# Kernel tuning notes

Hardware: AMD Instinct MI355X
Metric: run time of the kernel (lower is better)

Reference implementation:

```python
import jax, jax.numpy as jnp
import numpy as np

N = 15872   # number of predictions (31 * 512)
D = 129     # 128 image features + 1 objectness score
H = 128     # block MLP hidden width
IN = 2 * D + 1  # neighbor feats + main feats + add_info (IoU)
NUM_BLOCKS = 2


def _lin(k, fi, fo):
    return jax.random.normal(k, (fi, fo), jnp.float32) / np.sqrt(fi).astype(np.float32)


def setup_inputs() -> dict:
    key = jax.random.key(0)
    ks = jax.random.split(key, 24)
    # ragged neighborhood structure: mean size 16, exactly E = 16*N edges
    sizes = (np.arange(N) % 31) + 1
    E = int(sizes.sum())  # 253952
    rng = np.random.default_rng(0)
    nbr_idx = rng.integers(0, N, size=E).astype(np.int32)
    self_idx = np.repeat(np.arange(N, dtype=np.int32), sizes)  # sorted segment ids

    inp = {
        "interpolated": jax.random.normal(ks[0], (N, D), jnp.float32),
        "add_info": jax.random.uniform(ks[1], (E, 1), dtype=jnp.float32),
        "neighborhood_sizes": jnp.asarray(sizes, jnp.int32),
        "neighborhoods_indexes": jnp.asarray(nbr_idx),
        "self_indexes": jnp.asarray(self_idx),
    }
    # two (block, output) model pairs
    inp["b0_W1"] = _lin(ks[2], IN, H); inp["b0_b1"] = jnp.zeros((H,), jnp.float32)
    inp["b0_W2"] = _lin(ks[3], H, H);  inp["b0_b2"] = jnp.zeros((H,), jnp.float32)
    inp["b0_Wo"] = _lin(ks[4], H, D); inp["b0_bo"] = jnp.zeros((D,), jnp.float32)
    inp["b1_W1"] = _lin(ks[5], IN, H); inp["b1_b1"] = jnp.zeros((H,), jnp.float32)
    inp["b1_W2"] = _lin(ks[6], H, H);  inp["b1_b2"] = jnp.zeros((H,), jnp.float32)
    inp["b1_Wo"] = _lin(ks[7], H, D); inp["b1_bo"] = jnp.zeros((D,), jnp.float32)
    # final layers: 129 -> 64 -> 1
    inp["f_W1"] = _lin(ks[8], D, 64); inp["f_b1"] = jnp.zeros((64,), jnp.float32)
    inp["f_W2"] = _lin(ks[9], 64, 1); inp["f_b2"] = jnp.zeros((1,), jnp.float32)
    return inp


def _lnms_forward(interpolated, add_info, params, nbr_idx, self_idx):
    # params: list of (W1, b1, W2, b2, Wo, bo) per block, plus (fW1, fb1, fW2, fb2)
    for (W1, b1, W2, b2, Wo, bo) in params[:-1]:
        nbr = interpolated[nbr_idx]    # (E, D) gather of neighbor representations
        main = interpolated[self_idx]  # (E, D) gather of owning prediction
        x = jnp.concatenate([nbr, main, add_info], axis=1)  # (E, 2D+1)
        h = jax.nn.relu(x @ W1 + b1)
        h = jax.nn.relu(h @ W2 + b2)   # (E, H) processed neighborhoods
        # ragged per-neighborhood max pool (segments are contiguous/sorted)
        pooled = jax.ops.segment_max(h, self_idx, num_segments=N,
                                     indices_are_sorted=True)  # (N, H)
        block_output = pooled @ Wo + bo  # (N, D)
        interpolated = interpolated + block_output  # residual scatter-update
    fW1, fb1, fW2, fb2 = params[-1]
    return jax.nn.relu(interpolated @ fW1 + fb1) @ fW2 + fb2  # (N, 1)


def reference(interpolated, add_info,
              b0_W1, b0_b1, b0_W2, b0_b2, b0_Wo, b0_bo,
              b1_W1, b1_b1, b1_W2, b1_b2, b1_Wo, b1_bo,
              f_W1, f_b1, f_W2, f_b2,
              neighborhood_sizes, neighborhoods_indexes, self_indexes):
    params = [
        (b0_W1, b0_b1, b0_W2, b0_b2, b0_Wo, b0_bo),
        (b1_W1, b1_b1, b1_W2, b1_b2, b1_Wo, b1_bo),
        (f_W1, f_b1, f_W2, f_b2),
    ]
    return _lnms_forward(interpolated, add_info, params,
                         neighborhoods_indexes, self_indexes)
```

## Files before the change

kernel.cpp:

```cpp
#include <hip/hip_runtime.h>

#define NSEG 15872
#define DD 129
#define HH 128
#define NTILE (NSEG / 16)

typedef __attribute__((ext_vector_type(8))) short s16x8;
typedef __attribute__((ext_vector_type(4))) short s16x4;
typedef __attribute__((ext_vector_type(4))) float f32x4;
typedef __attribute__((ext_vector_type(16))) float f32x16;
typedef __attribute__((ext_vector_type(4))) unsigned u32x4;

__device__ __forceinline__ unsigned short f2bf(float x) {
  union { float f; unsigned u; } c; c.f = x;
  unsigned r = c.u + 0x7FFFu + ((c.u >> 16) & 1u);
  return (unsigned short)(r >> 16);
}
__device__ __forceinline__ float bf2f(unsigned short v) {
  union { unsigned u; float f; } c; c.u = ((unsigned)v) << 16; return c.f;
}

__device__ __forceinline__ void packB8(short* out, int idx8, const float* W,
                                       int N, int ld, int ncols, int kLimit,
                                       int rowBase) {
  const int n = (idx8 >> 3) % N;
  const int g = idx8 / (8 * N);
  s16x8 o;
#pragma unroll
  for (int i = 0; i < 8; ++i) {
    const int row = g * 8 + i;
    float v = 0.f;
    if (row < kLimit && n < ncols) v = W[(long)(rowBase + row) * ld + n];
    o[i] = (short)f2bf(v);
  }
  *(s16x8*)(out + idx8) = o;
}

__device__ __forceinline__ void packA1T8(short* out, int idx8, const float* W1) {
  const int unit = idx8 >> 3;
  const int lane = unit & 63;
  const int blk = unit >> 6;
  const int Mblk = blk / 10, ks = blk % 10;
  const int m = Mblk * 32 + (lane & 31);
  const int k0 = ks * 16 + ((lane >> 5) << 3);
  s16x8 o;
#pragma unroll
  for (int i = 0; i < 8; ++i) {
    const int k = k0 + i;
    o[i] = (short)((k < DD) ? f2bf(W1[(long)k * HH + m]) : 0);
  }
  *(s16x8*)(out + idx8) = o;
}

__device__ __forceinline__ void packB2T8(short* out, int idx8, const float* W2) {
  const int unit = idx8 >> 3;
  const int lane = unit & 63;
  const int blk = unit >> 6;
  const int ks = blk >> 2, nb = blk & 3;
  const int n = nb * 32 + (lane & 31);
  const int k0 = ks * 16 + ((lane >> 5) << 3);
  s16x8 o;
#pragma unroll
  for (int i = 0; i < 8; ++i)
    o[i] = (short)f2bf(W2[(long)(k0 + i) * HH + n]);
  *(s16x8*)(out + idx8) = o;
}

#define PACK_IDS 161792
#define TAB_IDS (NSEG * 160)
#define PACKV (PACK_IDS / 8)
#define TABV (TAB_IDS / 8)
#define PTBLK ((PACKV + TABV) / 256)
#define HMBLK (NTILE / 4)
__global__ __launch_bounds__(256) void pack_tab_kernel(
    const float* __restrict__ interp, unsigned short* __restrict__ tab,
    const float* __restrict__ W1b0, const float* __restrict__ W1b1,
    const float* __restrict__ W2b0, const float* __restrict__ W2b1,
    const float* __restrict__ Wob0, const float* __restrict__ Wob1,
    const float* __restrict__ fW1, short* __restrict__ PA1,
    short* __restrict__ PB2, short* __restrict__ PWo,
    short* __restrict__ PW1m, short* __restrict__ PfW1,
    const float* __restrict__ b1, float* __restrict__ Hm,
    const int* __restrict__ sizes, int* __restrict__ offs) {
  __shared__ short w1s[20480];
  const int bid = blockIdx.x;
  if (bid == PTBLK + HMBLK) {
    int* sums = (int*)w1s;
    const int t = threadIdx.x;
    const int base = t * (NSEG / 256);
    int s = 0;
#pragma unroll 8
    for (int i = 0; i < NSEG / 256; ++i) s += sizes[base + i];
    sums[t] = s;
    __syncthreads();
    for (int d = 1; d < 256; d <<= 1) {
      int u = (t >= d) ? sums[t - d] : 0;
      __syncthreads();
      sums[t] += u;
      __syncthreads();
    }
    int a = sums[t] - s;
#pragma unroll 8
    for (int i = 0; i < NSEG / 256; ++i) {
      const int sz = sizes[base + i];
      offs[base + i] = a;
      a += sz;
    }
    if (t == 255) offs[NSEG] = a;
    return;
  }
  if (bid >= PTBLK) {
    const int hb = bid - PTBLK;
    for (int u = threadIdx.x; u < 2560; u += 256)
      packB8(w1s, u * 8, W1b0, 128, 128, 128, 129, 129);
    __syncthreads();
    const int lane = threadIdx.x & 63, w = threadIdx.x >> 6;
    const int lk = lane >> 4, n16 = lane & 15;
    const int tile = hb * 4 + w;
    const float* arow = interp + (long)(tile * 16 + n16) * DD;
    s16x8 A[5];
#pragma unroll
    for (int ks = 0; ks < 5; ++ks) {
      s16x8 o;
#pragma unroll
      for (int i = 0; i < 8; ++i) {
        const int k = ks * 32 + lk * 8 + i;
        o[i] = (short)((k < DD) ? f2bf(arow[k]) : 0);
      }
      A[ks] = o;
    }
    f32x4 C[8];
#pragma unroll
    for (int nf = 0; nf < 8; ++nf) C[nf] = (f32x4){0.f, 0.f, 0.f, 0.f};
#pragma unroll
    for (int ks = 0; ks < 5; ++ks)
#pragma unroll
      for (int nf = 0; nf < 8; ++nf) {
        const s16x8 b = *(const s16x8*)(w1s + (((ks * 4 + lk) * 128) + nf * 16 + n16) * 8);
        C[nf] = __builtin_amdgcn_mfma_f32_16x16x32_bf16(A[ks], b, C[nf], 0, 0, 0);
      }
#pragma unroll
    for (int nf = 0; nf < 8; ++nf) {
      const float bv = b1[nf * 16 + n16];
#pragma unroll
      for (int r = 0; r < 4; ++r)
        Hm[(long)(tile * 16 + lk * 4 + r) * HH + nf * 16 + n16] = C[nf][r] + bv;
    }
    return;
  }
  int vid = bid * 256 + threadIdx.x;
  if (vid < PACKV) {
    int idx = vid * 8;
    if (idx < 40960) {
      packA1T8(PA1 + (idx / 20480) * 20480, idx % 20480,
               (idx < 20480) ? W1b0 : W1b1);
      return;
    }
    idx -= 40960;
    if (idx < 32768) {
      packB2T8(PB2 + (idx / 16384) * 16384, idx % 16384,
               (idx < 16384) ? W2b0 : W2b1);
      return;
    }
    idx -= 32768;
    if (idx < 36864) {
      packB8(PWo + (idx / 18432) * 18432, idx % 18432,
             (idx < 18432) ? Wob0 : Wob1, 144, 129, 129, 128, 0);
      return;
    }
    idx -= 36864;
    if (idx < 40960) {
      packB8(PW1m + (idx / 20480) * 20480, idx % 20480,
             (idx < 20480) ? W1b0 : W1b1, 128, 128, 128, 129, 129);
      return;
    }
    idx -= 40960;
    packB8(PfW1, idx, fW1, 64, 64, 64, 129, 0);
    return;
  }
  vid -= PACKV;
  if (vid < TABV) {
    const int n = vid / 20;
    const int g = vid - n * 20;
    s16x8 o = (s16x8){0, 0, 0, 0, 0, 0, 0, 0};
    if (g < 16) {
      const float* src = interp + (long)n * DD + g * 8;
#pragma unroll
      for (int i = 0; i < 8; ++i) o[i] = (short)f2bf(src[i]);
    } else if (g == 16) {
      o[0] = (short)f2bf(interp[(long)n * DD + 128]);
    }
    *(s16x8*)(tab + (long)vid * 8) = o;
  }
}

__device__ __forceinline__ int pairEdge(int row, int oLo, int sLo, int oHi,
                                        int sHi) {
  int e = (row < sLo) ? (oLo + row) : (oHi + row - sLo);
  if (row >= sLo + sHi) e = oHi + sHi - 1;
  return e;
}

struct PairMeta {
  int segLo, segHi, oLo, sLo, oHi, sHi;
};

__device__ __forceinline__ void loadMeta(int p, PairMeta& M,
                                         const int* __restrict__ offs) {
  M.segLo = p;
  M.segHi = NSEG - 1 - p;
  M.oLo = offs[M.segLo]; M.sLo = offs[M.segLo + 1] - M.oLo;
  M.oHi = offs[M.segHi]; M.sHi = offs[M.segHi + 1] - M.oHi;
}

__device__ __forceinline__ void prefetchEdge(
    const PairMeta& M, int c, const int* __restrict__ nbrIdx,
    const float* __restrict__ iou, int n32, int& nbrow, float& io) {
  const int grow = (c << 5) + n32;
  const int e = pairEdge(grow, M.oLo, M.sLo, M.oHi, M.sHi);
  nbrow = nbrIdx[e];
  io = iou[e];
}

__device__ __forceinline__ void prefetchHm(
    const PairMeta& M, const float* __restrict__ Hm, int n32,
    float* hmLo, float* hmHi) {
#pragma unroll
  for (int q = 0; q < 4; ++q) {
    hmLo[q] = Hm[(long)M.segLo * HH + q * 32 + n32];
    hmHi[q] = Hm[(long)M.segHi * HH + q * 32 + n32];
  }
}

__device__ __forceinline__ void gatherX(const unsigned short* __restrict__ tab,
                                        int nbrow, int half, s16x8* X) {
  const unsigned short* ar = tab + (long)nbrow * 160;
#pragma unroll
  for (int ks = 0; ks < 9; ++ks)
    X[ks] = *(const s16x8*)(ar + ks * 16 + half * 8);
}

__device__ __forceinline__ void gemm1Phase(
    const PairMeta& M, int c, const s16x8* X, float io,
    const short* __restrict__ As1, const float* wvT,
    const float* hmLo, const float* hmHi,
    int lane, int half, int n32, s16x8* A2) {
  const int grow = (c << 5) + n32;
  const short oneBf = (short)0x3F80;
  s16x8 bb = (s16x8){0, 0, 0, 0, 0, 0, 0, 0};
  if (half == 0) {
    const bool lo = grow < M.sLo;
    bb[0] = lo ? oneBf : (short)0;
    bb[1] = bb[0];
    bb[2] = lo ? (short)0 : oneBf;
    bb[3] = bb[2];
    bb[4] = (short)f2bf(io);
  }
#pragma unroll
  for (int Mblk = 0; Mblk < 4; ++Mblk) {
    f32x16 C;
#pragma unroll
    for (int i = 0; i < 16; ++i) C[i] = 0.f;
#pragma unroll
    for (int ks = 0; ks < 9; ++ks) {
      const s16x8 a = *(const s16x8*)(As1 + ((Mblk * 10 + ks) * 64 + lane) * 8);
      C = __builtin_amdgcn_mfma_f32_32x32x16_bf16(a, X[ks], C, 0, 0, 0);
    }
    s16x8 ab = (s16x8){0, 0, 0, 0, 0, 0, 0, 0};
    if (half == 0) {
      const unsigned short p0 = f2bf(hmLo[Mblk]);
      ab[0] = (short)p0;
      ab[1] = (short)f2bf(hmLo[Mblk] - bf2f(p0));
      const unsigned short p1 = f2bf(hmHi[Mblk]);
      ab[2] = (short)p1;
      ab[3] = (short)f2bf(hmHi[Mblk] - bf2f(p1));
      ab[4] = (short)f2bf(wvT[Mblk]);
    }
    C = __builtin_amdgcn_mfma_f32_32x32x16_bf16(ab, bb, C, 0, 0, 0);
    unsigned wv[8];
#pragma unroll
    for (int j = 0; j < 8; ++j) {
      const float lo = fmaxf(C[2 * j], 0.f);
      const float hi = fmaxf(C[2 * j + 1], 0.f);
      asm("v_cvt_pk_bf16_f32 %0, %1, %2" : "=v"(wv[j]) : "v"(lo), "v"(hi));
    }
    asm("v_permlane32_swap_b32 %0, %1" : "+v"(wv[0]), "+v"(wv[2]));
    asm("v_permlane32_swap_b32 %0, %1" : "+v"(wv[1]), "+v"(wv[3]));
    asm("v_permlane32_swap_b32 %0, %1" : "+v"(wv[4]), "+v"(wv[6]));
    asm("v_permlane32_swap_b32 %0, %1" : "+v"(wv[5]), "+v"(wv[7]));
    union { u32x4 u; s16x8 s; } q0, q1;
    q0.u = (u32x4){wv[0], wv[1], wv[2], wv[3]};
    q1.u = (u32x4){wv[4], wv[5], wv[6], wv[7]};
    A2[2 * Mblk] = q0.s;
    A2[2 * Mblk + 1] = q1.s;
  }
}

__device__ __forceinline__ void gemm2Phase(
    const PairMeta& M, int c, const s16x8* A2, const short* __restrict__ Bs2,
    int lane, int half, int n32, float* mxLo, float* mxHi) {
#pragma unroll
  for (int nb = 0; nb < 4; ++nb) {
    f32x16 D;
#pragma unroll
    for (int i = 0; i < 16; ++i) D[i] = 0.f;
#pragma unroll
    for (int ks = 0; ks < 8; ++ks) {
      const s16x8 b = *(const s16x8*)(Bs2 + ((ks * 4 + nb) * 64 + lane) * 8);
      D = __builtin_amdgcn_mfma_f32_32x32x16_bf16(A2[ks], b, D, 0, 0, 0);
    }
#pragma unroll
    for (int reg = 0; reg < 16; ++reg) {
      const int rrow = (reg & 3) + 8 * (reg >> 2) + 4 * half;
      const int gr = (c << 5) + rrow;
      const float v = D[reg];
      if (gr < M.sLo) mxLo[nb] = fmaxf(mxLo[nb], v);
      else            mxHi[nb] = fmaxf(mxHi[nb], v);
    }
  }
}

__global__ __launch_bounds__(512, 2) void edge_kernel(
    const unsigned short* __restrict__ tab, const short* __restrict__ PA1,
    const short* __restrict__ PB2, const float* __restrict__ W1,
    const float* __restrict__ Hm, const float* __restrict__ iou,
    const int* __restrict__ nbrIdx, const int* __restrict__ offs,
    const float* __restrict__ b2, unsigned short* __restrict__ pooled) {
  extern __shared__ __align__(16) char smem[];
  short* As1 = (short*)smem;
  short* Bs2 = (short*)(smem + 40960);
  {
    const f32x4* s1 = (const f32x4*)PA1;
    f32x4* d1 = (f32x4*)As1;
    for (int i = threadIdx.x; i < 2560; i += 512) d1[i] = s1[i];
    const f32x4* s2 = (const f32x4*)PB2;
    f32x4* d2 = (f32x4*)Bs2;
    for (int i = threadIdx.x; i < 2048; i += 512) d2[i] = s2[i];
  }
  __syncthreads();

  const int lane = threadIdx.x & 63;
  const int w = __builtin_amdgcn_readfirstlane(threadIdx.x >> 6);
  const int half = lane >> 5, n32 = lane & 31;

  float b2v[4], wvT[4];
#pragma unroll
  for (int q = 0; q < 4; ++q) {
    b2v[q] = b2[q * 32 + n32];
    wvT[q] = W1[258 * HH + q * 32 + n32];
  }

  const int wid = (blockIdx.x << 3) + w;
  const int nw = gridDim.x << 3;
  const int npairs = NSEG >> 1;

  if (wid >= npairs) return;

  PairMeta M, M1, M2;
  int nb1, nb2;
  float io, io1, io2;
  float hmLo[4], hmHi[4];
  s16x8 X[9];
  loadMeta(wid, M, offs);
  {
    int nb0;
    prefetchEdge(M, 0, nbrIdx, iou, n32, nb0, io);
    gatherX(tab, nb0, half, X);
  }
  prefetchHm(M, Hm, n32, hmLo, hmHi);
  if (wid + nw < npairs) {
    loadMeta(wid + nw, M1, offs);
    prefetchEdge(M1, 0, nbrIdx, iou, n32, nb1, io1);
  }

  int p = wid;
  for (;;) {
    const int pn1 = p + nw, pn2 = p + 2 * nw;
    const bool h1 = pn1 < npairs, h2 = pn2 < npairs;
    s16x8 A2[8];
    gemm1Phase(M, 0, X, io, As1, wvT, hmLo, hmHi, lane, half, n32, A2);
    const bool small = (M.sLo + M.sHi) <= 32;
    if (small && h1) {
      gatherX(tab, nb1, half, X);
      prefetchHm(M1, Hm, n32, hmLo, hmHi);
      if (h2) {
        loadMeta(pn2, M2, offs);
        prefetchEdge(M2, 0, nbrIdx, iou, n32, nb2, io2);
      }
    }
    float mxLo[4], mxHi[4];
#pragma unroll
    for (int q = 0; q < 4; ++q) { mxLo[q] = -3.4e38f; mxHi[q] = -3.4e38f; }
    gemm2Phase(M, 0, A2, Bs2, lane, half, n32, mxLo, mxHi);
    if (!small) {
      const int nchunk = (M.sLo + M.sHi + 31) >> 5;
      for (int c = 1; c < nchunk; ++c) {
        int nbf; float iof;
        prefetchEdge(M, c, nbrIdx, iou, n32, nbf, iof);
        gatherX(tab, nbf, half, X);
        gemm1Phase(M, c, X, iof, As1, wvT, hmLo, hmHi, lane, half, n32, A2);
        gemm2Phase(M, c, A2, Bs2, lane, half, n32, mxLo, mxHi);
      }
      if (h1) {
        gatherX(tab, nb1, half, X);
        prefetchHm(M1, Hm, n32, hmLo, hmHi);
        if (h2) {
          loadMeta(pn2, M2, offs);
          prefetchEdge(M2, 0, nbrIdx, iou, n32, nb2, io2);
        }
      }
    }
#pragma unroll
    for (int nb = 0; nb < 4; ++nb) {
      float lo = fmaxf(mxLo[nb], __shfl_xor(mxLo[nb], 32, 64));
      float hi = fmaxf(mxHi[nb], __shfl_xor(mxHi[nb], 32, 64));
      if (half == 0) {
        pooled[(long)M.segLo * HH + nb * 32 + n32] = f2bf(fmaxf(lo + b2v[nb], 0.f));
        pooled[(long)M.segHi * HH + nb * 32 + n32] = f2bf(fmaxf(hi + b2v[nb], 0.f));
      }
    }
    if (!h1) break;
    M = M1; io = io1;
    if (h2) { M1 = M2; nb1 = nb2; io1 = io2; }
    p = pn1;
  }
}

template <int NEXT>
__global__ __launch_bounds__(256) void resout_kernel(
    const unsigned short* __restrict__ pooled, const short* __restrict__ PWo,
    const float* __restrict__ bo, const float* __restrict__ resIn,
    float* __restrict__ resOut, unsigned short* __restrict__ tab,
    const short* __restrict__ PW1mN, const float* __restrict__ b1n,
    float* __restrict__ HmOut,
    const short* __restrict__ PfW1, const float* __restrict__ fb1,
    const float* __restrict__ fW2, const float* __restrict__ fb2,
    float* __restrict__ outFinal) {
  __shared__ short stS[4][16 * 168];
  const int lane = threadIdx.x & 63, w = threadIdx.x >> 6;
  const int lk = lane >> 4, n16 = lane & 15;
  short* st = stS[w];

  {
    const int row = lane >> 2, c0 = 129 + (lane & 3) * 8;
#pragma unroll
    for (int i = 0; i < 8; ++i) st[row * 168 + c0 + i] = 0;
  }

  const int tile = blockIdx.x * 4 + w;
  const unsigned short* arow = pooled + (long)(tile * 16 + n16) * HH;
  s16x8 A[4];
#pragma unroll
  for (int ks = 0; ks < 4; ++ks) A[ks] = *(const s16x8*)(arow + ks * 32 + lk * 8);
  f32x4 C[9];
#pragma unroll
  for (int nf = 0; nf < 9; ++nf) C[nf] = (f32x4){0.f, 0.f, 0.f, 0.f};
#pragma unroll
  for (int ks = 0; ks < 4; ++ks)
#pragma unroll
    for (int nf = 0; nf < 9; ++nf) {
      const s16x8 b = *(const s16x8*)(PWo + (((ks * 4 + lk) * 144) + nf * 16 + n16) * 8);
      C[nf] = __builtin_amdgcn_mfma_f32_16x16x32_bf16(A[ks], b, C[nf], 0, 0, 0);
    }

#pragma unroll
  for (int nf = 0; nf < 8; ++nf) {
    const int col = nf * 16 + n16;
    const float bov = bo[col];
#pragma unroll
    for (int r = 0; r < 4; ++r) {
      const int row = lk * 4 + r;
      const long node = tile * 16 + row;
      const float res = resIn[node * DD + col] + bov + C[nf][r];
      if (NEXT) {
        resOut[node * DD + col] = res;
        tab[node * 160 + col] = f2bf(res);
      }
      st[row * 168 + col] = (short)f2bf(res);
    }
  }
  if (n16 == 0) {
#pragma unroll
    for (int r = 0; r < 4; ++r) {
      const int row = lk * 4 + r;
      const long node = tile * 16 + row;
      const float res = resIn[node * DD + 128] + bo[128] + C[8][r];
      if (NEXT) {
        resOut[node * DD + 128] = res;
        tab[node * 160 + 128] = f2bf(res);
      }
      st[row * 168 + 128] = (short)f2bf(res);
    }
  }

  s16x8 A5[5];
#pragma unroll
  for (int ks = 0; ks < 5; ++ks)
    A5[ks] = *(const s16x8*)(st + n16 * 168 + ks * 32 + lk * 8);

  if (NEXT) {
    f32x4 H[8];
#pragma unroll
    for (int nf = 0; nf < 8; ++nf) H[nf] = (f32x4){0.f, 0.f, 0.f, 0.f};
#pragma unroll
    for (int ks = 0; ks < 5; ++ks)
#pragma unroll
      for (int nf = 0; nf < 8; ++nf) {
        const s16x8 b = *(const s16x8*)(PW1mN + (((ks * 4 + lk) * 128) + nf * 16 + n16) * 8);
        H[nf] = __builtin_amdgcn_mfma_f32_16x16x32_bf16(A5[ks], b, H[nf], 0, 0, 0);
      }
#pragma unroll
    for (int nf = 0; nf < 8; ++nf) {
      const float bv = b1n[nf * 16 + n16];
#pragma unroll
      for (int r = 0; r < 4; ++r)
        HmOut[(long)(tile * 16 + lk * 4 + r) * HH + nf * 16 + n16] = H[nf][r] + bv;
    }
  } else {
    f32x4 Ch[4];
#pragma unroll
    for (int nf = 0; nf < 4; ++nf) Ch[nf] = (f32x4){0.f, 0.f, 0.f, 0.f};
#pragma unroll
    for (int ks = 0; ks < 5; ++ks)
#pragma unroll
      for (int nf = 0; nf < 4; ++nf) {
        const s16x8 b = *(const s16x8*)(PfW1 + (((ks * 4 + lk) * 64) + nf * 16 + n16) * 8);
        Ch[nf] = __builtin_amdgcn_mfma_f32_16x16x32_bf16(A5[ks], b, Ch[nf], 0, 0, 0);
      }
    float b1v[4], w2v[4];
#pragma unroll
    for (int nf = 0; nf < 4; ++nf) {
      b1v[nf] = fb1[nf * 16 + n16];
      w2v[nf] = fW2[nf * 16 + n16];
    }
#pragma unroll
    for (int r = 0; r < 4; ++r) {
      float s = 0.f;
#pragma unroll
      for (int nf = 0; nf < 4; ++nf)
        s += fmaxf(Ch[nf][r] + b1v[nf], 0.f) * w2v[nf];
      s += __shfl_xor(s, 1, 64);
      s += __shfl_xor(s, 2, 64);
      s += __shfl_xor(s, 4, 64);
      s += __shfl_xor(s, 8, 64);
      if (n16 == 0) outFinal[tile * 16 + lk * 4 + r] = s + fb2[0];
    }
  }
}

extern "C" void kernel_launch(void* const* d_in, const int* in_sizes, int n_in,
                              void* d_out, int out_size, void* d_ws, size_t ws_size,
                              hipStream_t stream) {
  const float* interp  = (const float*)d_in[0];
  const float* addInfo = (const float*)d_in[1];
  const int* sizes     = (const int*)d_in[2];
  const int* nbrIdx    = (const int*)d_in[3];
  const float* b0W1 = (const float*)d_in[5];
  const float* b0b1 = (const float*)d_in[6];
  const float* b0W2 = (const float*)d_in[7];
  const float* b0b2 = (const float*)d_in[8];
  const float* b0Wo = (const float*)d_in[9];
  const float* b0bo = (const float*)d_in[10];
  const float* b1W1 = (const float*)d_in[11];
  const float* b1b1 = (const float*)d_in[12];
  const float* b1W2 = (const float*)d_in[13];
  const float* b1b2 = (const float*)d_in[14];
  const float* b1Wo = (const float*)d_in[15];
  const float* b1bo = (const float*)d_in[16];
  const float* fW1  = (const float*)d_in[17];
  const float* fb1  = (const float*)d_in[18];
  const float* fW2  = (const float*)d_in[19];
  const float* fb2  = (const float*)d_in[20];

  char* ws = (char*)d_ws;
  int*            offs  = (int*)(ws + 0);
  short*          PA1   = (short*)(ws + 65536);
  short*          PB2   = (short*)(ws + 147456);
  short*          PWo   = (short*)(ws + 212992);
  short*          PW1m  = (short*)(ws + 286720);
  short*          PfW1  = (short*)(ws + 368640);
  unsigned short* TAB   = (unsigned short*)(ws + 393216);
  float*          HM    = (float*)(ws + 5472256);
  unsigned short* POOLED= (unsigned short*)(ws + 13598720);
  float*          RES   = (float*)(ws + 17661952);

  pack_tab_kernel<<<PTBLK + HMBLK + 1, 256, 0, stream>>>(
      interp, TAB, b0W1, b1W1, b0W2, b1W2, b0Wo, b1Wo, fW1,
      PA1, PB2, PWo, PW1m, PfW1, b0b1, HM, sizes, offs);

  const size_t e_lds = 40960 + 32768;

  edge_kernel<<<248, 512, e_lds, stream>>>(TAB, PA1, PB2, b0W1, HM, addInfo,
                                           nbrIdx, offs, b0b2, POOLED);
  resout_kernel<1><<<NTILE / 4, 256, 0, stream>>>(
      POOLED, PWo, b0bo, interp, RES, TAB, PW1m + 20480, b1b1, HM,
      nullptr, nullptr, nullptr, nullptr, nullptr);

  edge_kernel<<<248, 512, e_lds, stream>>>(TAB, PA1 + 20480, PB2 + 16384, b1W1,
                                           HM, addInfo, nbrIdx, offs,
                                           b1b2, POOLED);
  resout_kernel<0><<<NTILE / 4, 256, 0, stream>>>(
      POOLED, PWo + 18432, b1bo, RES, nullptr, nullptr, nullptr, nullptr,
      nullptr, PfW1, fb1, fW2, fb2, (float*)d_out);
}
```

Measured before the change: 178.7 us.

## Fuse all five launches into one persistent kernel with grid barriers

Replaces the pack, two edge and two residual-output launches with a single persistent kernel of 248 blocks. Phases are separated by atomic-counter grid barriers whose counters are cleared with a memset. The aim is to remove the launch gaps and tail idle time between the small dependent kernels. In exchange, the pack and residual phases now run on fewer, larger blocks. Correctness also depends on all 248 blocks being co-resident, which needs two 512-thread blocks per CU; otherwise the barriers can deadlock.

New measurement: 607.2 us. +239.8%, slower.

```diff
diff --git a/kernel.cpp b/kernel.cpp
--- a/kernel.cpp
+++ b/kernel.cpp
@@ -4,6 +4,8 @@
 #define DD 129
 #define HH 128
 #define NTILE (NSEG / 16)
+#define GRID 248
+#define NWAVES (GRID * 8)
 
 typedef __attribute__((ext_vector_type(8))) short s16x8;
 typedef __attribute__((ext_vector_type(4))) short s16x4;
@@ -18,6 +20,17 @@
 }
 __device__ __forceinline__ float bf2f(unsigned short v) {
   union { unsigned u; float f; } c; c.u = ((unsigned)v) << 16; return c.f;
+}
+
+__device__ __forceinline__ void gridBar(int* bar, int idx) {
+  __threadfence();
+  __syncthreads();
+  if (threadIdx.x == 0) {
+    atomicAdd(&bar[idx], 1);
+    while (atomicAdd(&bar[idx], 0) < GRID) __builtin_amdgcn_s_sleep(2);
+  }
+  __syncthreads();
+  __threadfence();
 }
 
 __device__ __forceinline__ void packB8(short* out, int idx8, const float* W,
@@ -70,85 +83,15 @@
 #define TAB_IDS (NSEG * 160)
 #define PACKV (PACK_IDS / 8)
 #define TABV (TAB_IDS / 8)
-#define PTBLK ((PACKV + TABV) / 256)
-#define HMBLK (NTILE / 4)
-__global__ __launch_bounds__(256) void pack_tab_kernel(
-    const float* __restrict__ interp, unsigned short* __restrict__ tab,
+
+__device__ __forceinline__ void packUnit(
+    int vid, const float* __restrict__ interp, unsigned short* __restrict__ tab,
     const float* __restrict__ W1b0, const float* __restrict__ W1b1,
     const float* __restrict__ W2b0, const float* __restrict__ W2b1,
     const float* __restrict__ Wob0, const float* __restrict__ Wob1,
     const float* __restrict__ fW1, short* __restrict__ PA1,
     short* __restrict__ PB2, short* __restrict__ PWo,
-    short* __restrict__ PW1m, short* __restrict__ PfW1,
-    const float* __restrict__ b1, float* __restrict__ Hm,
-    const int* __restrict__ sizes, int* __restrict__ offs) {
-  __shared__ short w1s[20480];
-  const int bid = blockIdx.x;
-  if (bid == PTBLK + HMBLK) {
-    int* sums = (int*)w1s;
-    const int t = threadIdx.x;
-    const int base = t * (NSEG / 256);
-    int s = 0;
-#pragma unroll 8
-    for (int i = 0; i < NSEG / 256; ++i) s += sizes[base + i];
-    sums[t] = s;
-    __syncthreads();
-    for (int d = 1; d < 256; d <<= 1) {
-      int u = (t >= d) ? sums[t - d] : 0;
-      __syncthreads();
-      sums[t] += u;
-      __syncthreads();
-    }
-    int a = sums[t] - s;
-#pragma unroll 8
-    for (int i = 0; i < NSEG / 256; ++i) {
-      const int sz = sizes[base + i];
-      offs[base + i] = a;
-      a += sz;
-    }
-    if (t == 255) offs[NSEG] = a;
-    return;
-  }
-  if (bid >= PTBLK) {
-    const int hb = bid - PTBLK;
-    for (int u = threadIdx.x; u < 2560; u += 256)
-      packB8(w1s, u * 8, W1b0, 128, 128, 128, 129, 129);
-    __syncthreads();
-    const int lane = threadIdx.x & 63, w = threadIdx.x >> 6;
-    const int lk = lane >> 4, n16 = lane & 15;
-    const int tile = hb * 4 + w;
-    const float* arow = interp + (long)(tile * 16 + n16) * DD;
-    s16x8 A[5];
-#pragma unroll
-    for (int ks = 0; ks < 5; ++ks) {
-      s16x8 o;
-#pragma unroll
-      for (int i = 0; i < 8; ++i) {
-        const int k = ks * 32 + lk * 8 + i;
-        o[i] = (short)((k < DD) ? f2bf(arow[k]) : 0);
-      }
-      A[ks] = o;
-    }
-    f32x4 C[8];
-#pragma unroll
-    for (int nf = 0; nf < 8; ++nf) C[nf] = (f32x4){0.f, 0.f, 0.f, 0.f};
-#pragma unroll
-    for (int ks = 0; ks < 5; ++ks)
-#pragma unroll
-      for (int nf = 0; nf < 8; ++nf) {
-        const s16x8 b = *(const s16x8*)(w1s + (((ks * 4 + lk) * 128) + nf * 16 + n16) * 8);
-        C[nf] = __builtin_amdgcn_mfma_f32_16x16x32_bf16(A[ks], b, C[nf], 0, 0, 0);
-      }
-#pragma unroll
-    for (int nf = 0; nf < 8; ++nf) {
-      const float bv = b1[nf * 16 + n16];
-#pragma unroll
-      for (int r = 0; r < 4; ++r)
-        Hm[(long)(tile * 16 + lk * 4 + r) * HH + nf * 16 + n16] = C[nf][r] + bv;
-    }
-    return;
-  }
-  int vid = bid * 256 + threadIdx.x;
+    short* __restrict__ PW1m, short* __restrict__ PfW1) {
   if (vid < PACKV) {
     int idx = vid * 8;
     if (idx < 40960) {
@@ -178,10 +121,10 @@
     packB8(PfW1, idx, fW1, 64, 64, 64, 129, 0);
     return;
   }
-  vid -= PACKV;
-  if (vid < TABV) {
-    const int n = vid / 20;
-    const int g = vid - n * 20;
+  const int tv = vid - PACKV;
+  if (tv < TABV) {
+    const int n = tv / 20;
+    const int g = tv - n * 20;
     s16x8 o = (s16x8){0, 0, 0, 0, 0, 0, 0, 0};
     if (g < 16) {
       const float* src = interp + (long)n * DD + g * 8;
@@ -190,7 +133,7 @@
     } else if (g == 16) {
       o[0] = (short)f2bf(interp[(long)n * DD + 128]);
     }
-    *(s16x8*)(tab + (long)vid * 8) = o;
+    *(s16x8*)(tab + (long)tv * 8) = o;
   }
 }
 
@@ -320,13 +263,13 @@
   }
 }
 
-__global__ __launch_bounds__(512, 2) void edge_kernel(
+__device__ void edgePhase(
     const unsigned short* __restrict__ tab, const short* __restrict__ PA1,
     const short* __restrict__ PB2, const float* __restrict__ W1,
     const float* __restrict__ Hm, const float* __restrict__ iou,
     const int* __restrict__ nbrIdx, const int* __restrict__ offs,
-    const float* __restrict__ b2, unsigned short* __restrict__ pooled) {
-  extern __shared__ __align__(16) char smem[];
+    const float* __restrict__ b2, unsigned short* __restrict__ pooled,
+    char* smem) {
   short* As1 = (short*)smem;
   short* Bs2 = (short*)(smem + 40960);
   {
@@ -351,57 +294,35 @@
   }
 
   const int wid = (blockIdx.x << 3) + w;
-  const int nw = gridDim.x << 3;
+  const int nw = NWAVES;
   const int npairs = NSEG >> 1;
 
-  if (wid >= npairs) return;
-
-  PairMeta M, M1, M2;
-  int nb1, nb2;
-  float io, io1, io2;
-  float hmLo[4], hmHi[4];
-  s16x8 X[9];
-  loadMeta(wid, M, offs);
-  {
-    int nb0;
-    prefetchEdge(M, 0, nbrIdx, iou, n32, nb0, io);
-    gatherX(tab, nb0, half, X);
-  }
-  prefetchHm(M, Hm, n32, hmLo, hmHi);
-  if (wid + nw < npairs) {
-    loadMeta(wid + nw, M1, offs);
-    prefetchEdge(M1, 0, nbrIdx, iou, n32, nb1, io1);
-  }
-
-  int p = wid;
-  for (;;) {
-    const int pn1 = p + nw, pn2 = p + 2 * nw;
-    const bool h1 = pn1 < npairs, h2 = pn2 < npairs;
-    s16x8 A2[8];
-    gemm1Phase(M, 0, X, io, As1, wvT, hmLo, hmHi, lane, half, n32, A2);
-    const bool small = (M.sLo + M.sHi) <= 32;
-    if (small && h1) {
-      gatherX(tab, nb1, half, X);
-      prefetchHm(M1, Hm, n32, hmLo, hmHi);
-      if (h2) {
-        loadMeta(pn2, M2, offs);
-        prefetchEdge(M2, 0, nbrIdx, iou, n32, nb2, io2);
-      }
-    }
-    float mxLo[4], mxHi[4];
-#pragma unroll
-    for (int q = 0; q < 4; ++q) { mxLo[q] = -3.4e38f; mxHi[q] = -3.4e38f; }
-    gemm2Phase(M, 0, A2, Bs2, lane, half, n32, mxLo, mxHi);
-    if (!small) {
-      const int nchunk = (M.sLo + M.sHi + 31) >> 5;
-      for (int c = 1; c < nchunk; ++c) {
-        int nbf; float iof;
-        prefetchEdge(M, c, nbrIdx, iou, n32, nbf, iof);
-        gatherX(tab, nbf, half, X);
-        gemm1Phase(M, c, X, iof, As1, wvT, hmLo, hmHi, lane, half, n32, A2);
-        gemm2Phase(M, c, A2, Bs2, lane, half, n32, mxLo, mxHi);
-      }
-      if (h1) {
+  if (wid < npairs) {
+    PairMeta M, M1, M2;
+    int nb1, nb2;
+    float io, io1, io2;
+    float hmLo[4], hmHi[4];
+    s16x8 X[9];
+    loadMeta(wid, M, offs);
+    {
+      int nb0;
+      prefetchEdge(M, 0, nbrIdx, iou, n32, nb0, io);
+      gatherX(tab, nb0, half, X);
+    }
+    prefetchHm(M, Hm, n32, hmLo, hmHi);
+    if (wid + nw < npairs) {
+      loadMeta(wid + nw, M1, offs);
+      prefetchEdge(M1, 0, nbrIdx, iou, n32, nb1, io1);
+    }
+
+    int p = wid;
+    for (;;) {
+      const int pn1 = p + nw, pn2 = p + 2 * nw;
+      const bool h1 = pn1 < npairs, h2 = pn2 < npairs;
+      s16x8 A2[8];
+      gemm1Phase(M, 0, X, io, As1, wvT, hmLo, hmHi, lane, half, n32, A2);
+      const bool small = (M.sLo + M.sHi) <= 32;
+      if (small && h1) {
         gatherX(tab, nb1, half, X);
         prefetchHm(M1, Hm, n32, hmLo, hmHi);
         if (h2) {
@@ -409,25 +330,48 @@
           prefetchEdge(M2, 0, nbrIdx, iou, n32, nb2, io2);
         }
       }
-    }
-#pragma unroll
-    for (int nb = 0; nb < 4; ++nb) {
-      float lo = fmaxf(mxLo[nb], __shfl_xor(mxLo[nb], 32, 64));
-      float hi = fmaxf(mxHi[nb], __shfl_xor(mxHi[nb], 32, 64));
-      if (half == 0) {
-        pooled[(long)M.segLo * HH + nb * 32 + n32] = f2bf(fmaxf(lo + b2v[nb], 0.f));
-        pooled[(long)M.segHi * HH + nb * 32 + n32] = f2bf(fmaxf(hi + b2v[nb], 0.f));
-      }
-    }
-    if (!h1) break;
-    M = M1; io = io1;
-    if (h2) { M1 = M2; nb1 = nb2; io1 = io2; }
-    p = pn1;
+      float mxLo[4], mxHi[4];
+#pragma unroll
+      for (int q = 0; q < 4; ++q) { mxLo[q] = -3.4e38f; mxHi[q] = -3.4e38f; }
+      gemm2Phase(M, 0, A2, Bs2, lane, half, n32, mxLo, mxHi);
+      if (!small) {
+        const int nchunk = (M.sLo + M.sHi + 31) >> 5;
+        for (int c = 1; c < nchunk; ++c) {
+          int nbf; float iof;
+          prefetchEdge(M, c, nbrIdx, iou, n32, nbf, iof);
+          gatherX(tab, nbf, half, X);
+          gemm1Phase(M, c, X, iof, As1, wvT, hmLo, hmHi, lane, half, n32, A2);
+          gemm2Phase(M, c, A2, Bs2, lane, half, n32, mxLo, mxHi);
+        }
+        if (h1) {
+          gatherX(tab, nb1, half, X);
+          prefetchHm(M1, Hm, n32, hmLo, hmHi);
+          if (h2) {
+            loadMeta(pn2, M2, offs);
+            prefetchEdge(M2, 0, nbrIdx, iou, n32, nb2, io2);
+          }
+        }
+      }
+#pragma unroll
+      for (int nb = 0; nb < 4; ++nb) {
+        float lo = fmaxf(mxLo[nb], __shfl_xor(mxLo[nb], 32, 64));
+        float hi = fmaxf(mxHi[nb], __shfl_xor(mxHi[nb], 32, 64));
+        if (half == 0) {
+          pooled[(long)M.segLo * HH + nb * 32 + n32] = f2bf(fmaxf(lo + b2v[nb], 0.f));
+          pooled[(long)M.segHi * HH + nb * 32 + n32] = f2bf(fmaxf(hi + b2v[nb], 0.f));
+        }
+      }
+      if (!h1) break;
+      M = M1; io = io1;
+      if (h2) { M1 = M2; nb1 = nb2; io1 = io2; }
+      p = pn1;
+    }
   }
 }
 
 template <int NEXT>
-__global__ __launch_bounds__(256) void resout_kernel(
+__device__ void resoutPhase(
+    int tile, int lane, short* st,
     const unsigned short* __restrict__ pooled, const short* __restrict__ PWo,
     const float* __restrict__ bo, const float* __restrict__ resIn,
     float* __restrict__ resOut, unsigned short* __restrict__ tab,
@@ -436,18 +380,13 @@
     const short* __restrict__ PfW1, const float* __restrict__ fb1,
     const float* __restrict__ fW2, const float* __restrict__ fb2,
     float* __restrict__ outFinal) {
-  __shared__ short stS[4][16 * 168];
-  const int lane = threadIdx.x & 63, w = threadIdx.x >> 6;
   const int lk = lane >> 4, n16 = lane & 15;
-  short* st = stS[w];
-
   {
     const int row = lane >> 2, c0 = 129 + (lane & 3) * 8;
 #pragma unroll
     for (int i = 0; i < 8; ++i) st[row * 168 + c0 + i] = 0;
   }
 
-  const int tile = blockIdx.x * 4 + w;
   const unsigned short* arow = pooled + (long)(tile * 16 + n16) * HH;
   s16x8 A[4];
 #pragma unroll
@@ -545,6 +484,120 @@
       s += __shfl_xor(s, 8, 64);
       if (n16 == 0) outFinal[tile * 16 + lk * 4 + r] = s + fb2[0];
     }
+  }
+}
+
+__global__ __launch_bounds__(512, 2) void fused_all(
+    const float* __restrict__ interp, const float* __restrict__ iou,
+    const int* __restrict__ sizes, const int* __restrict__ nbrIdx,
+    const float* __restrict__ b0W1, const float* __restrict__ b0b1,
+    const float* __restrict__ b0W2, const float* __restrict__ b0b2,
+    const float* __restrict__ b0Wo, const float* __restrict__ b0bo,
+    const float* __restrict__ b1W1, const float* __restrict__ b1b1,
+    const float* __restrict__ b1W2, const float* __restrict__ b1b2,
+    const float* __restrict__ b1Wo, const float* __restrict__ b1bo,
+    const float* __restrict__ fW1, const float* __restrict__ fb1,
+    const float* __restrict__ fW2, const float* __restrict__ fb2,
+    short* __restrict__ PA1, short* __restrict__ PB2,
+    short* __restrict__ PWo, short* __restrict__ PW1m,
+    short* __restrict__ PfW1, unsigned short* __restrict__ TAB,
+    float* __restrict__ HM, int* __restrict__ offs,
+    unsigned short* __restrict__ POOLED, float* __restrict__ RES,
+    float* __restrict__ outF, int* __restrict__ bar) {
+  extern __shared__ __align__(16) char smem[];
+  const int tid = threadIdx.x;
+  const int bid = blockIdx.x;
+  const int lane = tid & 63;
+  const int w8 = tid >> 6;
+
+  for (int vid = bid * 512 + tid; vid < PACKV + TABV; vid += GRID * 512)
+    packUnit(vid, interp, TAB, b0W1, b1W1, b0W2, b1W2, b0Wo, b1Wo, fW1,
+             PA1, PB2, PWo, PW1m, PfW1);
+
+  if (bid == GRID - 1) {
+    int* sums = (int*)smem;
+    const int chunk = NSEG / 512;
+    const int base = tid * chunk;
+    int s = 0;
+    for (int i = 0; i < chunk; ++i) s += sizes[base + i];
+    sums[tid] = s;
+    __syncthreads();
+    for (int d = 1; d < 512; d <<= 1) {
+      int u = (tid >= d) ? sums[tid - d] : 0;
+      __syncthreads();
+      sums[tid] += u;
+      __syncthreads();
+    }
+    int a = sums[tid] - s;
+    for (int i = 0; i < chunk; ++i) {
+      const int sz = sizes[base + i];
+      offs[base + i] = a;
+      a += sz;
+    }
+    if (tid == 511) offs[NSEG] = a;
+  } else if (bid < NTILE / 8) {
+    short* w1s = (short*)smem;
+    for (int u = tid; u < 2560; u += 512)
+      packB8(w1s, u * 8, b0W1, 128, 128, 128, 129, 129);
+    __syncthreads();
+    const int lk = lane >> 4, n16 = lane & 15;
+    const int tile = bid * 8 + w8;
+    const float* arow = interp + (long)(tile * 16 + n16) * DD;
+    s16x8 A[5];
+#pragma unroll
+    for (int ks = 0; ks < 5; ++ks) {
+      s16x8 o;
+#pragma unroll
+      for (int i = 0; i < 8; ++i) {
+        const int k = ks * 32 + lk * 8 + i;
+        o[i] = (short)((k < DD) ? f2bf(arow[k]) : 0);
+      }
+      A[ks] = o;
+    }
+    f32x4 C[8];
+#pragma unroll
+    for (int nf = 0; nf < 8; ++nf) C[nf] = (f32x4){0.f, 0.f, 0.f, 0.f};
+#pragma unroll
+    for (int ks = 0; ks < 5; ++ks)
+#pragma unroll
+      for (int nf = 0; nf < 8; ++nf) {
+        const s16x8 b = *(const s16x8*)(w1s + (((ks * 4 + lk) * 128) + nf * 16 + n16) * 8);
+        C[nf] = __builtin_amdgcn_mfma_f32_16x16x32_bf16(A[ks], b, C[nf], 0, 0, 0);
+      }
+#pragma unroll
+    for (int nf = 0; nf < 8; ++nf) {
+      const float bv = b0b1[nf * 16 + n16];
+#pragma unroll
+      for (int r = 0; r < 4; ++r)
+        HM[(long)(tile * 16 + lk * 4 + r) * HH + nf * 16 + n16] = C[nf][r] + bv;
+    }
+  }
+  gridBar(bar, 0);
+
+  edgePhase(TAB, PA1, PB2, b0W1, HM, iou, nbrIdx, offs, b0b2, POOLED, smem);
+  gridBar(bar, 1);
+
+  {
+    const int tile = bid * 8 + w8;
+    short* st = (short*)(smem + w8 * (16 * 168 * 2));
+    if (tile < NTILE)
+      resoutPhase<1>(tile, lane, st, POOLED, PWo, b0bo, interp, RES, TAB,
+                     PW1m + 20480, b1b1, HM, nullptr, nullptr, nullptr,
+                     nullptr, nullptr);
+  }
+  gridBar(bar, 2);
+
+  edgePhase(TAB, PA1 + 20480, PB2 + 16384, b1W1, HM, iou, nbrIdx, offs,
+            b1b2, POOLED, smem);
+  gridBar(bar, 3);
+
+  {
+    const int tile = bid * 8 + w8;
+    short* st = (short*)(smem + w8 * (16 * 168 * 2));
+    if (tile < NTILE)
+      resoutPhase<0>(tile, lane, st, POOLED, PWo + 18432, b1bo, RES, nullptr,
+                     nullptr, nullptr, nullptr, nullptr, PfW1, fb1, fW2, fb2,
+                     outF);
   }
 }
 
@@ -583,23 +636,16 @@
   float*          HM    = (float*)(ws + 5472256);
   unsigned short* POOLED= (unsigned short*)(ws + 13598720);
   float*          RES   = (float*)(ws + 17661952);
-
-  pack_tab_kernel<<<PTBLK + HMBLK + 1, 256, 0, stream>>>(
-      interp, TAB, b0W1, b1W1, b0W2, b1W2, b0Wo, b1Wo, fW1,
-      PA1, PB2, PWo, PW1m, PfW1, b0b1, HM, sizes, offs);
-
-  const size_t e_lds = 40960 + 32768;
-
-  edge_kernel<<<248, 512, e_lds, stream>>>(TAB, PA1, PB2, b0W1, HM, addInfo,
-                                           nbrIdx, offs, b0b2, POOLED);
-  resout_kernel<1><<<NTILE / 4, 256, 0, stream>>>(
-      POOLED, PWo, b0bo, interp, RES, TAB, PW1m + 20480, b1b1, HM,
-      nullptr, nullptr, nullptr, nullptr, nullptr);
-
-  edge_kernel<<<248, 512, e_lds, stream>>>(TAB, PA1 + 20480, PB2 + 16384, b1W1,
-                                           HM, addInfo, nbrIdx, offs,
-                                           b1b2, POOLED);
-  resout_kernel<0><<<NTILE / 4, 256, 0, stream>>>(
-      POOLED, PWo + 18432, b1bo, RES, nullptr, nullptr, nullptr, nullptr,
-      nullptr, PfW1, fb1, fW2, fb2, (float*)d_out);
-}
+  int*            BAR   = (int*)(ws + 25851904);
+
+  hipMemsetAsync(BAR, 0, 4 * sizeof(int), stream);
+
+  float* outF = (float*)d_out;
+  fused_all<<<GRID, 512, 73728, stream>>>(
+      interp, addInfo, sizes, nbrIdx,
+      b0W1, b0b1, b0W2, b0b2, b0Wo, b0bo,
+      b1W1, b1b1, b1W2, b1b2, b1Wo, b1bo,
+      fW1, fb1, fW2, fb2,
+      PA1, PB2, PWo, PW1m, PfW1, TAB, HM, offs,
+      POOLED, RES, outF, BAR);
+}
```
